# Kernel tuning notes

Hardware: AMD Instinct MI355X
Metric: run time of the kernel (lower is better)

The kernel has to match this reference:

```python
import jax, jax.numpy as jnp
import numpy as np

U, I, NG, D, G, B = 100000, 50000, 20000, 64, 20, 16384
H_GE = (D + 2 * D) // 2  # 96, group_encoder hidden

def setup_inputs() -> dict:
    key = jax.random.key(0)
    ks = jax.random.split(key, 24)
    s = 0.1
    return {
        'group_inputs': jax.random.randint(ks[0], (B,), 0, NG),
        'item_inputs': jax.random.randint(ks[1], (B,), 0, I),
        'group_members': jax.random.randint(ks[2], (NG, G), 0, U),
        'eps': jax.random.normal(ks[3], (B, D), dtype=jnp.float32),
        'user_emb': jax.random.normal(ks[4], (U, D), dtype=jnp.float32) * s,
        'item_emb': jax.random.normal(ks[5], (I, D), dtype=jnp.float32) * s,
        # user_encoder: MLP(D, D, 1) -> Linear(D,D), ReLU, Linear(D,D)
        'ue_w1': jax.random.normal(ks[6], (D, D), dtype=jnp.float32) * s,
        'ue_b1': jnp.zeros((D,), jnp.float32),
        'ue_w2': jax.random.normal(ks[7], (D, D), dtype=jnp.float32) * s,
        'ue_b2': jnp.zeros((D,), jnp.float32),
        # group_encoder: MLP(D, 2D, 1) -> Linear(D,96), ReLU, Linear(96,2D)
        'ge_w1': jax.random.normal(ks[8], (D, H_GE), dtype=jnp.float32) * s,
        'ge_b1': jnp.zeros((H_GE,), jnp.float32),
        'ge_w2': jax.random.normal(ks[9], (H_GE, 2 * D), dtype=jnp.float32) * s,
        'ge_b2': jnp.zeros((2 * D,), jnp.float32),
        # attention: Linear(2D,16), ReLU, Linear(16,1)
        'at_w1': jax.random.normal(ks[10], (2 * D, 16), dtype=jnp.float32) * s,
        'at_b1': jnp.zeros((16,), jnp.float32),
        'at_w2': jax.random.normal(ks[11], (16, 1), dtype=jnp.float32) * s,
        'at_b2': jnp.zeros((1,), jnp.float32),
        # predict: Linear(3D,8), ReLU, Linear(8,1)
        'pr_w1': jax.random.normal(ks[12], (3 * D, 8), dtype=jnp.float32) * s,
        'pr_b1': jnp.zeros((8,), jnp.float32),
        'pr_w2': jax.random.normal(ks[13], (8, 1), dtype=jnp.float32) * s,
        'pr_b2': jnp.zeros((1,), jnp.float32),
    }

def reference(group_inputs, item_inputs, group_members, eps,
              user_emb, item_emb,
              ue_w1, ue_b1, ue_w2, ue_b2,
              ge_w1, ge_b1, ge_w2, ge_b2,
              at_w1, at_b1, at_w2, at_b2,
              pr_w1, pr_b1, pr_w2, pr_b2):
    mem_idx = group_members[group_inputs]              # [B, G]
    me = user_emb[mem_idx]                             # [B, G, D] gather
    # user encoder MLP
    enc = jnp.maximum(me @ ue_w1 + ue_b1, 0) @ ue_w2 + ue_b2
    gz = jnp.maximum(jnp.mean(enc, axis=1), 0)         # [B, D]
    gz = jnp.maximum(gz @ ge_w1 + ge_b1, 0) @ ge_w2 + ge_b2  # [B, 2D]
    z_mu, log_sigma = gz[:, :D], gz[:, D:]
    z_sigma = 0.1 + 0.9 * jax.nn.sigmoid(log_sigma)
    ie = item_emb[item_inputs]                          # [B, D]
    gi = jnp.concatenate([me, jnp.broadcast_to(ie[:, None, :], me.shape)], axis=-1)  # [B, G, 2D]
    score = jnp.maximum(gi @ at_w1 + at_b1, 0) @ at_w2 + at_b2  # [B, G, 1]
    w = jax.nn.softmax(score[..., 0], axis=1)           # [B, G]
    g_att = jnp.einsum('bg,bgd->bd', w, me)             # [B, D]
    ge_full = g_att + z_mu + z_sigma * eps              # sample_z with given eps
    ncf = jnp.concatenate([ge_full * ie, ge_full, ie], axis=-1)  # [B, 3D]
    h = jnp.maximum(ncf @ pr_w1 + pr_b1, 0) @ pr_w2 + pr_b2
    return jax.nn.sigmoid(h)                            # [B, 1]
```

## Files before the change

kernel.cpp:

```cpp
#include <hip/hip_runtime.h>
#include <hip/hip_bf16.h>
#include <math.h>

#define G_   20
#define BT   16

typedef __attribute__((ext_vector_type(8))) short bf8;
typedef __attribute__((ext_vector_type(4))) float f4;

#define FMB  0
#define FAT  10
#define FUE2 12
#define FGE1 20
#define FGE2 32
#define FPR  56
#define FTOT 62

__device__ __forceinline__ unsigned cvt2(float x, float y){
    float2 f; f.x = x; f.y = y;
    __hip_bfloat162 h = __float22bfloat162_rn(f);
    return *reinterpret_cast<unsigned*>(&h);
}
__device__ __forceinline__ unsigned short cvt1(float x){
    __hip_bfloat16 h = __float2bfloat16(x);
    return *reinterpret_cast<unsigned short*>(&h);
}
__device__ __forceinline__ bf8 pack8(float4 a, float4 b){
    union { bf8 v; unsigned u[4]; } t;
    t.u[0] = cvt2(a.x, a.y); t.u[1] = cvt2(a.z, a.w);
    t.u[2] = cvt2(b.x, b.y); t.u[3] = cvt2(b.z, b.w);
    return t.v;
}

__global__ __launch_bounds__(256) void vargr_prep(
    const float* __restrict__ ue_w1, const float* __restrict__ ue_w2,
    const float* __restrict__ ge_w1, const float* __restrict__ ge_w2,
    const float* __restrict__ at_w1, const float* __restrict__ pr_w1,
    unsigned short* __restrict__ ws)
{
    int f = blockIdx.x * 256 + threadIdx.x;
    if (f >= FTOT * 64) return;
    int lane = f & 63, grp = f >> 6;
    int col = lane & 15;
    int q8  = (lane >> 4) * 8;
    float v[8];
    if (grp < FAT){
        int g = grp - FMB; int nt = g >> 1; int k0 = (g & 1)*32 + q8; int c = nt*16 + col;
        #pragma unroll
        for (int q = 0; q < 8; ++q)
            v[q] = (c < 64) ? ue_w1[(k0+q)*64 + c] : at_w1[(k0+q)*16 + (c - 64)];
    } else if (grp < FUE2){
        int g = grp - FAT; int k0 = g*32 + q8;
        #pragma unroll
        for (int q = 0; q < 8; ++q) v[q] = at_w1[(64 + k0 + q)*16 + col];
    } else if (grp < FGE1){
        int g = grp - FUE2; int nt = g >> 1; int k0 = (g & 1)*32 + q8;
        #pragma unroll
        for (int q = 0; q < 8; ++q) v[q] = ue_w2[(k0+q)*64 + nt*16 + col];
    } else if (grp < FGE2){
        int g = grp - FGE1; int nt = g >> 1; int k0 = (g & 1)*32 + q8;
        #pragma unroll
        for (int q = 0; q < 8; ++q) v[q] = ge_w1[(k0+q)*96 + nt*16 + col];
    } else if (grp < FPR){
        int g = grp - FGE2; int nt = g / 3; int k0 = (g % 3)*32 + q8;
        #pragma unroll
        for (int q = 0; q < 8; ++q) v[q] = ge_w2[(k0+q)*128 + nt*16 + col];
    } else {
        int g = grp - FPR; int k0 = g*32 + q8;
        #pragma unroll
        for (int q = 0; q < 8; ++q) v[q] = (col < 8) ? pr_w1[(k0+q)*8 + col] : 0.f;
    }
    union { bf8 b; unsigned u[4]; } t;
    t.u[0] = cvt2(v[0], v[1]); t.u[1] = cvt2(v[2], v[3]);
    t.u[2] = cvt2(v[4], v[5]); t.u[3] = cvt2(v[6], v[7]);
    *reinterpret_cast<bf8*>(ws + (size_t)f * 8) = t.b;
}

__global__ __launch_bounds__(256, 2) void vargr_main(
    const int*   __restrict__ group_inputs,
    const int*   __restrict__ item_inputs,
    const int*   __restrict__ group_members,
    const float* __restrict__ eps,
    const float* __restrict__ user_emb,
    const float* __restrict__ item_emb,
    const float* __restrict__ ue_b1, const float* __restrict__ ue_b2,
    const float* __restrict__ ge_b1, const float* __restrict__ ge_b2,
    const float* __restrict__ at_b1, const float* __restrict__ at_w2,
    const float* __restrict__ at_b2, const float* __restrict__ pr_b1,
    const float* __restrict__ pr_w2, const float* __restrict__ pr_b2,
    const unsigned short* __restrict__ ws,
    float* __restrict__ out)
{
    __shared__ unsigned short xAh[BT*136];
    __shared__ unsigned short xBh[BT*136];
    __shared__ float ieb[BT*68];
    __shared__ float gefb[BT*64];
    __shared__ float wsm[BT*G_];
    __shared__ int   sidx[BT*G_];
    __shared__ float x3u[BT*132];

    const int tid = threadIdx.x;
    const int w = tid >> 6, l = tid & 63;
    const int lq = l >> 4, lr = l & 15;
    const int bbase = blockIdx.x * BT;
    const bf8* wsf = (const bf8*)ws;

    bf8 bfr[5][2];
    #pragma unroll
    for (int nt = 0; nt < 5; ++nt)
        #pragma unroll
        for (int kt = 0; kt < 2; ++kt)
            bfr[nt][kt] = wsf[(FMB + nt*2 + kt)*64 + l];
    bf8 abot0 = wsf[(FAT + 0)*64 + l];
    bf8 abot1 = wsf[(FAT + 1)*64 + l];

    float bias1[4];
    #pragma unroll
    for (int nt = 0; nt < 4; ++nt) bias1[nt] = ue_b1[nt*16 + lr];
    const float aw2  = at_w2[lr];
    const float atb2 = at_b2[0];

    {
        int bb = 4*w + lq;
        int item = item_inputs[bbase + bb];
        ((float4*)(ieb + bb*68))[lr] = ((const float4*)(item_emb + (size_t)item*64))[lr];
    }
    if (l < G_){
        #pragma unroll
        for (int i = 0; i < 4; ++i){
            int bb = 4*w + i;
            int gid = group_inputs[bbase + bb];
            sidx[bb*G_ + l] = group_members[gid*G_ + l];
        }
    }
    __syncthreads();

    float4 r0, r1, r2, r3;
    {
        int sx = sidx[(4*w + (lr >> 2))*G_ + 16 + (lr & 3)];
        const float4* p = (const float4*)(user_emb + (size_t)sx*64) + lq*2;
        r0 = p[0]; r1 = p[1]; r2 = p[8]; r3 = p[9];
    }
    float4 c0, c1, c2, c3;
    {
        int sx = sidx[(4*w + 0)*G_ + lr];
        const float4* p = (const float4*)(user_emb + (size_t)sx*64) + lq*2;
        c0 = p[0]; c1 = p[1]; c2 = p[8]; c3 = p[9];
    }

    f4 tvacc = (f4){0.f, 0.f, 0.f, 0.f};
    #pragma unroll
    for (int kt = 0; kt < 2; ++kt){
        const float* ap = ieb + lr*68 + kt*32 + lq*8;
        bf8 a = pack8(*(const float4*)ap, *(const float4*)(ap + 4));
        tvacc = __builtin_amdgcn_mfma_f32_16x16x32_bf16(a, kt ? abot1 : abot0, tvacc, 0, 0, 0);
    }
    const float atb1 = at_b1[lr];
    float tvi[4];
    #pragma unroll
    for (int i = 0; i < 4; ++i)
        tvi[i] = __shfl(tvacc[i], w*16 + lr) + atb1;

    float rem[4];
    {
        bf8 a0 = pack8(r0, r1);
        bf8 a1 = pack8(r2, r3);
        f4 acc[5];
        #pragma unroll
        for (int nt = 0; nt < 5; ++nt) acc[nt] = (f4){0.f, 0.f, 0.f, 0.f};
        #pragma unroll
        for (int nt = 0; nt < 5; ++nt){
            acc[nt] = __builtin_amdgcn_mfma_f32_16x16x32_bf16(a0, bfr[nt][0], acc[nt], 0, 0, 0);
            acc[nt] = __builtin_amdgcn_mfma_f32_16x16x32_bf16(a1, bfr[nt][1], acc[nt], 0, 0, 0);
        }
        #pragma unroll
        for (int nt = 0; nt < 4; ++nt){
            float rs = 0.f;
            #pragma unroll
            for (int rr = 0; rr < 4; ++rr) rs += fmaxf(acc[nt][rr] + bias1[nt], 0.f);
            rem[nt] = rs;
        }
        float tvq = (lq == 0) ? tvi[0] : (lq == 1) ? tvi[1] : (lq == 2) ? tvi[2] : tvi[3];
        float vv[4];
        #pragma unroll
        for (int rr = 0; rr < 4; ++rr) vv[rr] = fmaxf(acc[4][rr] + tvq, 0.f) * aw2;
        #pragma unroll
        for (int rr = 0; rr < 4; ++rr){
            vv[rr] += __shfl_xor(vv[rr], 1, 16);
            vv[rr] += __shfl_xor(vv[rr], 2, 16);
            vv[rr] += __shfl_xor(vv[rr], 4, 16);
            vv[rr] += __shfl_xor(vv[rr], 8, 16);
        }
        if (lr == 0){
            #pragma unroll
            for (int rr = 0; rr < 4; ++rr)
                wsm[(4*w + lq)*G_ + 16 + rr] = vv[rr] + atb2;
        }
    }

    #pragma unroll
    for (int i = 0; i < 4; ++i){
        float4 n0, n1, n2, n3;
        if (i < 3){
            int sx = sidx[(4*w + i + 1)*G_ + lr];
            const float4* p = (const float4*)(user_emb + (size_t)sx*64) + lq*2;
            n0 = p[0]; n1 = p[1]; n2 = p[8]; n3 = p[9];
        }
        const int bb = 4*w + i;
        bf8 a0 = pack8(c0, c1);
        bf8 a1 = pack8(c2, c3);
        f4 acc[5];
        #pragma unroll
        for (int nt = 0; nt < 5; ++nt) acc[nt] = (f4){0.f, 0.f, 0.f, 0.f};
        #pragma unroll
        for (int nt = 0; nt < 5; ++nt){
            acc[nt] = __builtin_amdgcn_mfma_f32_16x16x32_bf16(a0, bfr[nt][0], acc[nt], 0, 0, 0);
            acc[nt] = __builtin_amdgcn_mfma_f32_16x16x32_bf16(a1, bfr[nt][1], acc[nt], 0, 0, 0);
        }
        #pragma unroll
        for (int nt = 0; nt < 4; ++nt){
            float rs = 0.f;
            #pragma unroll
            for (int rr = 0; rr < 4; ++rr) rs += fmaxf(acc[nt][rr] + bias1[nt], 0.f);
            if (lq == i) rs += rem[nt];
            rs += __shfl_xor(rs, 16);
            rs += __shfl_xor(rs, 32);
            if (lq == nt) xAh[bb*136 + nt*16 + lr] = cvt1(rs * (1.f / G_));
        }
        {
            float vv[4];
            #pragma unroll
            for (int rr = 0; rr < 4; ++rr) vv[rr] = fmaxf(acc[4][rr] + tvi[i], 0.f) * aw2;
            #pragma unroll
            for (int rr = 0; rr < 4; ++rr){
                vv[rr] += __shfl_xor(vv[rr], 1, 16);
                vv[rr] += __shfl_xor(vv[rr], 2, 16);
                vv[rr] += __shfl_xor(vv[rr], 4, 16);
                vv[rr] += __shfl_xor(vv[rr], 8, 16);
            }
            if (lr == 0){
                #pragma unroll
                for (int rr = 0; rr < 4; ++rr)
                    wsm[bb*G_ + 4*lq + rr] = vv[rr] + atb2;
            }
        }
        {
            float sval = (l < G_) ? wsm[bb*G_ + l] : -3.0e38f;
            float mx = sval;
            mx = fmaxf(mx, __shfl_xor(mx, 1, 32));
            mx = fmaxf(mx, __shfl_xor(mx, 2, 32));
            mx = fmaxf(mx, __shfl_xor(mx, 4, 32));
            mx = fmaxf(mx, __shfl_xor(mx, 8, 32));
            mx = fmaxf(mx, __shfl_xor(mx, 16, 32));
            float e = (l < G_) ? expf(sval - mx) : 0.f;
            float sm = e;
            sm += __shfl_xor(sm, 1, 32);
            sm += __shfl_xor(sm, 2, 32);
            sm += __shfl_xor(sm, 4, 32);
            sm += __shfl_xor(sm, 8, 32);
            sm += __shfl_xor(sm, 16, 32);
            if (l < G_) wsm[bb*G_ + l] = e / sm;
        }
        {
            float ga = 0.f;
            #pragma unroll
            for (int g = 0; g < G_; ++g)
                ga += wsm[bb*G_ + g] * user_emb[(size_t)sidx[bb*G_ + g]*64 + l];
            gefb[bb*64 + l] = ga;
        }
        c0 = n0; c1 = n1; c2 = n2; c3 = n3;
    }

    __syncthreads();
    if (w != 0) return;

    float ev[16];
    #pragma unroll
    for (int bb = 0; bb < BT; ++bb)
        ev[bb] = eps[(size_t)(bbase + bb)*64 + l];

    #pragma unroll
    for (int nt = 0; nt < 4; ++nt){
        int col = nt*16 + lr;
        f4 acc = (f4){0.f, 0.f, 0.f, 0.f};
        #pragma unroll
        for (int kt = 0; kt < 2; ++kt){
            bf8 a = *(const bf8*)(xAh + lr*136 + kt*32 + lq*8);
            acc = __builtin_amdgcn_mfma_f32_16x16x32_bf16(a, wsf[(FUE2 + nt*2 + kt)*64 + l], acc, 0, 0, 0);
        }
        float bs = ue_b2[col];
        #pragma unroll
        for (int rr = 0; rr < 4; ++rr)
            xBh[(4*lq + rr)*136 + col] = cvt1(fmaxf(acc[rr] + bs, 0.f));
    }
    #pragma unroll
    for (int t = 0; t < 6; ++t){
        int col = t*16 + lr;
        f4 acc = (f4){0.f, 0.f, 0.f, 0.f};
        #pragma unroll
        for (int kt = 0; kt < 2; ++kt){
            bf8 a = *(const bf8*)(xBh + lr*136 + kt*32 + lq*8);
            acc = __builtin_amdgcn_mfma_f32_16x16x32_bf16(a, wsf[(FGE1 + t*2 + kt)*64 + l], acc, 0, 0, 0);
        }
        float bs = ge_b1[col];
        #pragma unroll
        for (int rr = 0; rr < 4; ++rr)
            xAh[(4*lq + rr)*136 + col] = cvt1(fmaxf(acc[rr] + bs, 0.f));
    }
    #pragma unroll
    for (int t = 0; t < 8; ++t){
        int col = t*16 + lr;
        f4 acc = (f4){0.f, 0.f, 0.f, 0.f};
        #pragma unroll
        for (int kt = 0; kt < 3; ++kt){
            bf8 a = *(const bf8*)(xAh + lr*136 + kt*32 + lq*8);
            acc = __builtin_amdgcn_mfma_f32_16x16x32_bf16(a, wsf[(FGE2 + t*3 + kt)*64 + l], acc, 0, 0, 0);
        }
        float bs = ge_b2[col];
        #pragma unroll
        for (int rr = 0; rr < 4; ++rr)
            x3u[(4*lq + rr)*132 + col] = acc[rr] + bs;
    }

    float gefv[BT];
    #pragma unroll
    for (int bb = 0; bb < BT; ++bb){
        float mu  = x3u[bb*132 + l];
        float sgr = x3u[bb*132 + 64 + l];
        float sg  = 0.1f + 0.9f / (1.f + expf(-sgr));
        gefv[bb] = gefb[bb*64 + l] + mu + sg * ev[bb];
    }
    asm volatile("" ::: "memory");
    unsigned short* ncf = (unsigned short*)x3u;
    #pragma unroll
    for (int bb = 0; bb < BT; ++bb){
        float gef = gefv[bb];
        float iev = ieb[bb*68 + l];
        ncf[bb*200 + l]       = cvt1(gef * iev);
        ncf[bb*200 + 64 + l]  = cvt1(gef);
        ncf[bb*200 + 128 + l] = cvt1(iev);
    }
    {
        f4 acc = (f4){0.f, 0.f, 0.f, 0.f};
        #pragma unroll
        for (int kt = 0; kt < 6; ++kt){
            bf8 a = *(const bf8*)(ncf + lr*200 + kt*32 + lq*8);
            acc = __builtin_amdgcn_mfma_f32_16x16x32_bf16(a, wsf[(FPR + kt)*64 + l], acc, 0, 0, 0);
        }
        float pb1 = (lr < 8) ? pr_b1[lr] : 0.f;
        float pw2 = (lr < 8) ? pr_w2[lr] : 0.f;
        float pb2 = pr_b2[0];
        float vv[4];
        #pragma unroll
        for (int rr = 0; rr < 4; ++rr) vv[rr] = fmaxf(acc[rr] + pb1, 0.f) * pw2;
        #pragma unroll
        for (int rr = 0; rr < 4; ++rr){
            vv[rr] += __shfl_xor(vv[rr], 1, 16);
            vv[rr] += __shfl_xor(vv[rr], 2, 16);
            vv[rr] += __shfl_xor(vv[rr], 4, 16);
            vv[rr] += __shfl_xor(vv[rr], 8, 16);
        }
        if (lr == 0){
            #pragma unroll
            for (int rr = 0; rr < 4; ++rr)
                out[bbase + 4*lq + rr] = 1.f / (1.f + expf(-(vv[rr] + pb2)));
        }
    }
}

extern "C" void kernel_launch(void* const* d_in, const int* in_sizes, int n_in,
                              void* d_out, int out_size, void* d_ws, size_t ws_size,
                              hipStream_t stream) {
    const int*   group_inputs  = (const int*)d_in[0];
    const int*   item_inputs   = (const int*)d_in[1];
    const int*   group_members = (const int*)d_in[2];
    const float* eps           = (const float*)d_in[3];
    const float* user_emb      = (const float*)d_in[4];
    const float* item_emb      = (const float*)d_in[5];
    const float* ue_w1 = (const float*)d_in[6];
    const float* ue_b1 = (const float*)d_in[7];
    const float* ue_w2 = (const float*)d_in[8];
    const float* ue_b2 = (const float*)d_in[9];
    const float* ge_w1 = (const float*)d_in[10];
    const float* ge_b1 = (const float*)d_in[11];
    const float* ge_w2 = (const float*)d_in[12];
    const float* ge_b2 = (const float*)d_in[13];
    const float* at_w1 = (const float*)d_in[14];
    const float* at_b1 = (const float*)d_in[15];
    const float* at_w2 = (const float*)d_in[16];
    const float* at_b2 = (const float*)d_in[17];
    const float* pr_w1 = (const float*)d_in[18];
    const float* pr_b1 = (const float*)d_in[19];
    const float* pr_w2 = (const float*)d_in[20];
    const float* pr_b2 = (const float*)d_in[21];
    float* out = (float*)d_out;
    unsigned short* ws = (unsigned short*)d_ws;

    vargr_prep<<<(FTOT*64 + 255)/256, 256, 0, stream>>>(
        ue_w1, ue_w2, ge_w1, ge_w2, at_w1, pr_w1, ws);

    const int nb = in_sizes[0];
    vargr_main<<<nb / BT, 256, 0, stream>>>(
        group_inputs, item_inputs, group_members, eps, user_emb, item_emb,
        ue_b1, ue_b2, ge_b1, ge_b2, at_b1, at_w2, at_b2, pr_b1, pr_w2, pr_b2,
        ws, out);
}
```

Measured before the change: 40.07 us.

## Split main kernel into gather phase and separate parallel MLP tail kernel

The fused kernel is split in two. The first kernel does the gather, the user-encoder first layer and the attention, and writes the mean hidden, the attended embedding and the item embeddings to workspace. The second kernel runs the group encoder and predict MLPs with every wave active, instead of only wave 0 after a barrier as before. This removes the serial tail where three of four waves sat idle. In exchange it adds an extra launch and round-trips the intermediates through global memory.

Result: slower. 44.72 us (+11.6%).

```diff
diff --git a/kernel.cpp b/kernel.cpp
--- a/kernel.cpp
+++ b/kernel.cpp
@@ -15,6 +15,9 @@
 #define FGE2 32
 #define FPR  56
 #define FTOT 62
+#define HBAR_BOFF  65536u
+#define GEF_BOFF   2162688u
+#define IE_BOFF    6356992u
 
 __device__ __forceinline__ unsigned cvt2(float x, float y){
     float2 f; f.x = x; f.y = y;
@@ -76,28 +79,22 @@
     *reinterpret_cast<bf8*>(ws + (size_t)f * 8) = t.b;
 }
 
-__global__ __launch_bounds__(256, 2) void vargr_main(
+__global__ __launch_bounds__(256, 2) void vargr_phase1(
     const int*   __restrict__ group_inputs,
     const int*   __restrict__ item_inputs,
     const int*   __restrict__ group_members,
-    const float* __restrict__ eps,
     const float* __restrict__ user_emb,
     const float* __restrict__ item_emb,
-    const float* __restrict__ ue_b1, const float* __restrict__ ue_b2,
-    const float* __restrict__ ge_b1, const float* __restrict__ ge_b2,
-    const float* __restrict__ at_b1, const float* __restrict__ at_w2,
-    const float* __restrict__ at_b2, const float* __restrict__ pr_b1,
-    const float* __restrict__ pr_w2, const float* __restrict__ pr_b2,
+    const float* __restrict__ ue_b1, const float* __restrict__ at_b1,
+    const float* __restrict__ at_w2, const float* __restrict__ at_b2,
     const unsigned short* __restrict__ ws,
-    float* __restrict__ out)
+    unsigned short* __restrict__ hbar,
+    float* __restrict__ gef,
+    float* __restrict__ iebuf)
 {
-    __shared__ unsigned short xAh[BT*136];
-    __shared__ unsigned short xBh[BT*136];
     __shared__ float ieb[BT*68];
-    __shared__ float gefb[BT*64];
     __shared__ float wsm[BT*G_];
     __shared__ int   sidx[BT*G_];
-    __shared__ float x3u[BT*132];
 
     const int tid = threadIdx.x;
     const int w = tid >> 6, l = tid & 63;
@@ -123,7 +120,9 @@
     {
         int bb = 4*w + lq;
         int item = item_inputs[bbase + bb];
-        ((float4*)(ieb + bb*68))[lr] = ((const float4*)(item_emb + (size_t)item*64))[lr];
+        float4 v = ((const float4*)(item_emb + (size_t)item*64))[lr];
+        ((float4*)(ieb + bb*68))[lr] = v;
+        ((float4*)(iebuf + (size_t)(bbase + bb)*64))[lr] = v;
     }
     if (l < G_){
         #pragma unroll
@@ -225,7 +224,7 @@
             if (lq == i) rs += rem[nt];
             rs += __shfl_xor(rs, 16);
             rs += __shfl_xor(rs, 32);
-            if (lq == nt) xAh[bb*136 + nt*16 + lr] = cvt1(rs * (1.f / G_));
+            if (lq == nt) hbar[(size_t)(bbase + bb)*64 + nt*16 + lr] = cvt1(rs * (1.f / G_));
         }
         {
             float vv[4];
@@ -266,79 +265,102 @@
             #pragma unroll
             for (int g = 0; g < G_; ++g)
                 ga += wsm[bb*G_ + g] * user_emb[(size_t)sidx[bb*G_ + g]*64 + l];
-            gefb[bb*64 + l] = ga;
+            gef[(size_t)(bbase + bb)*64 + l] = ga;
         }
         c0 = n0; c1 = n1; c2 = n2; c3 = n3;
     }
-
-    __syncthreads();
-    if (w != 0) return;
+}
+
+__global__ __launch_bounds__(128) void vargr_tail(
+    const float* __restrict__ eps,
+    const float* __restrict__ ue_b2, const float* __restrict__ ge_b1,
+    const float* __restrict__ ge_b2, const float* __restrict__ pr_b1,
+    const float* __restrict__ pr_w2, const float* __restrict__ pr_b2,
+    const unsigned short* __restrict__ ws,
+    const unsigned short* __restrict__ hbar,
+    const float* __restrict__ gef,
+    const float* __restrict__ iebuf,
+    float* __restrict__ out)
+{
+    __shared__ unsigned short xA[2][16*136];
+    __shared__ unsigned short xB[2][16*136];
+    __shared__ float x3[2][16*132];
+
+    const int tid = threadIdx.x;
+    const int w = tid >> 6, l = tid & 63;
+    const int lq = l >> 4, lr = l & 15;
+    const int m0 = blockIdx.x * 32 + w * 16;
+    const bf8* wsf = (const bf8*)ws;
 
     float ev[16];
     #pragma unroll
-    for (int bb = 0; bb < BT; ++bb)
-        ev[bb] = eps[(size_t)(bbase + bb)*64 + l];
+    for (int j = 0; j < 16; ++j)
+        ev[j] = eps[(size_t)(m0 + j)*64 + l];
+
+    bf8 ha0 = *(const bf8*)(hbar + (size_t)(m0 + lr)*64 + 0  + lq*8);
+    bf8 ha1 = *(const bf8*)(hbar + (size_t)(m0 + lr)*64 + 32 + lq*8);
 
     #pragma unroll
     for (int nt = 0; nt < 4; ++nt){
         int col = nt*16 + lr;
         f4 acc = (f4){0.f, 0.f, 0.f, 0.f};
-        #pragma unroll
-        for (int kt = 0; kt < 2; ++kt){
-            bf8 a = *(const bf8*)(xAh + lr*136 + kt*32 + lq*8);
-            acc = __builtin_amdgcn_mfma_f32_16x16x32_bf16(a, wsf[(FUE2 + nt*2 + kt)*64 + l], acc, 0, 0, 0);
-        }
+        acc = __builtin_amdgcn_mfma_f32_16x16x32_bf16(ha0, wsf[(FUE2 + nt*2 + 0)*64 + l], acc, 0, 0, 0);
+        acc = __builtin_amdgcn_mfma_f32_16x16x32_bf16(ha1, wsf[(FUE2 + nt*2 + 1)*64 + l], acc, 0, 0, 0);
         float bs = ue_b2[col];
         #pragma unroll
         for (int rr = 0; rr < 4; ++rr)
-            xBh[(4*lq + rr)*136 + col] = cvt1(fmaxf(acc[rr] + bs, 0.f));
-    }
-    #pragma unroll
-    for (int t = 0; t < 6; ++t){
-        int col = t*16 + lr;
-        f4 acc = (f4){0.f, 0.f, 0.f, 0.f};
-        #pragma unroll
-        for (int kt = 0; kt < 2; ++kt){
-            bf8 a = *(const bf8*)(xBh + lr*136 + kt*32 + lq*8);
-            acc = __builtin_amdgcn_mfma_f32_16x16x32_bf16(a, wsf[(FGE1 + t*2 + kt)*64 + l], acc, 0, 0, 0);
-        }
-        float bs = ge_b1[col];
-        #pragma unroll
-        for (int rr = 0; rr < 4; ++rr)
-            xAh[(4*lq + rr)*136 + col] = cvt1(fmaxf(acc[rr] + bs, 0.f));
-    }
-    #pragma unroll
-    for (int t = 0; t < 8; ++t){
-        int col = t*16 + lr;
-        f4 acc = (f4){0.f, 0.f, 0.f, 0.f};
-        #pragma unroll
-        for (int kt = 0; kt < 3; ++kt){
-            bf8 a = *(const bf8*)(xAh + lr*136 + kt*32 + lq*8);
-            acc = __builtin_amdgcn_mfma_f32_16x16x32_bf16(a, wsf[(FGE2 + t*3 + kt)*64 + l], acc, 0, 0, 0);
-        }
-        float bs = ge_b2[col];
-        #pragma unroll
-        for (int rr = 0; rr < 4; ++rr)
-            x3u[(4*lq + rr)*132 + col] = acc[rr] + bs;
-    }
-
-    float gefv[BT];
-    #pragma unroll
-    for (int bb = 0; bb < BT; ++bb){
-        float mu  = x3u[bb*132 + l];
-        float sgr = x3u[bb*132 + 64 + l];
+            xB[w][(4*lq + rr)*136 + col] = cvt1(fmaxf(acc[rr] + bs, 0.f));
+    }
+    {
+        bf8 ga0 = *(const bf8*)(&xB[w][lr*136 + 0  + lq*8]);
+        bf8 ga1 = *(const bf8*)(&xB[w][lr*136 + 32 + lq*8]);
+        #pragma unroll
+        for (int t = 0; t < 6; ++t){
+            int col = t*16 + lr;
+            f4 acc = (f4){0.f, 0.f, 0.f, 0.f};
+            acc = __builtin_amdgcn_mfma_f32_16x16x32_bf16(ga0, wsf[(FGE1 + t*2 + 0)*64 + l], acc, 0, 0, 0);
+            acc = __builtin_amdgcn_mfma_f32_16x16x32_bf16(ga1, wsf[(FGE1 + t*2 + 1)*64 + l], acc, 0, 0, 0);
+            float bs = ge_b1[col];
+            #pragma unroll
+            for (int rr = 0; rr < 4; ++rr)
+                xA[w][(4*lq + rr)*136 + col] = cvt1(fmaxf(acc[rr] + bs, 0.f));
+        }
+    }
+    {
+        bf8 ta0 = *(const bf8*)(&xA[w][lr*136 + 0  + lq*8]);
+        bf8 ta1 = *(const bf8*)(&xA[w][lr*136 + 32 + lq*8]);
+        bf8 ta2 = *(const bf8*)(&xA[w][lr*136 + 64 + lq*8]);
+        #pragma unroll
+        for (int t = 0; t < 8; ++t){
+            int col = t*16 + lr;
+            f4 acc = (f4){0.f, 0.f, 0.f, 0.f};
+            acc = __builtin_amdgcn_mfma_f32_16x16x32_bf16(ta0, wsf[(FGE2 + t*3 + 0)*64 + l], acc, 0, 0, 0);
+            acc = __builtin_amdgcn_mfma_f32_16x16x32_bf16(ta1, wsf[(FGE2 + t*3 + 1)*64 + l], acc, 0, 0, 0);
+            acc = __builtin_amdgcn_mfma_f32_16x16x32_bf16(ta2, wsf[(FGE2 + t*3 + 2)*64 + l], acc, 0, 0, 0);
+            float bs = ge_b2[col];
+            #pragma unroll
+            for (int rr = 0; rr < 4; ++rr)
+                x3[w][(4*lq + rr)*132 + col] = acc[rr] + bs;
+        }
+    }
+
+    float gefv[16];
+    #pragma unroll
+    for (int j = 0; j < 16; ++j){
+        float mu  = x3[w][j*132 + l];
+        float sgr = x3[w][j*132 + 64 + l];
         float sg  = 0.1f + 0.9f / (1.f + expf(-sgr));
-        gefv[bb] = gefb[bb*64 + l] + mu + sg * ev[bb];
+        gefv[j] = gef[(size_t)(m0 + j)*64 + l] + mu + sg * ev[j];
     }
     asm volatile("" ::: "memory");
-    unsigned short* ncf = (unsigned short*)x3u;
-    #pragma unroll
-    for (int bb = 0; bb < BT; ++bb){
-        float gef = gefv[bb];
-        float iev = ieb[bb*68 + l];
-        ncf[bb*200 + l]       = cvt1(gef * iev);
-        ncf[bb*200 + 64 + l]  = cvt1(gef);
-        ncf[bb*200 + 128 + l] = cvt1(iev);
+    unsigned short* ncf = (unsigned short*)&x3[w][0];
+    #pragma unroll
+    for (int j = 0; j < 16; ++j){
+        float g  = gefv[j];
+        float ie = iebuf[(size_t)(m0 + j)*64 + l];
+        ncf[j*200 + l]       = cvt1(g * ie);
+        ncf[j*200 + 64 + l]  = cvt1(g);
+        ncf[j*200 + 128 + l] = cvt1(ie);
     }
     {
         f4 acc = (f4){0.f, 0.f, 0.f, 0.f};
@@ -363,7 +385,7 @@
         if (lr == 0){
             #pragma unroll
             for (int rr = 0; rr < 4; ++rr)
-                out[bbase + 4*lq + rr] = 1.f / (1.f + expf(-(vv[rr] + pb2)));
+                out[m0 + 4*lq + rr] = 1.f / (1.f + expf(-(vv[rr] + pb2)));
         }
     }
 }
@@ -396,12 +418,19 @@
     float* out = (float*)d_out;
     unsigned short* ws = (unsigned short*)d_ws;
 
+    unsigned short* hbar  = (unsigned short*)((char*)d_ws + HBAR_BOFF);
+    float*          gef   = (float*)((char*)d_ws + GEF_BOFF);
+    float*          iebuf = (float*)((char*)d_ws + IE_BOFF);
+
     vargr_prep<<<(FTOT*64 + 255)/256, 256, 0, stream>>>(
         ue_w1, ue_w2, ge_w1, ge_w2, at_w1, pr_w1, ws);
 
     const int nb = in_sizes[0];
-    vargr_main<<<nb / BT, 256, 0, stream>>>(
-        group_inputs, item_inputs, group_members, eps, user_emb, item_emb,
-        ue_b1, ue_b2, ge_b1, ge_b2, at_b1, at_w2, at_b2, pr_b1, pr_w2, pr_b2,
-        ws, out);
-}
+    vargr_phase1<<<nb / BT, 256, 0, stream>>>(
+        group_inputs, item_inputs, group_members, user_emb, item_emb,
+        ue_b1, at_b1, at_w2, at_b2, ws, hbar, gef, iebuf);
+
+    vargr_tail<<<nb / 32, 128, 0, stream>>>(
+        eps, ue_b2, ge_b1, ge_b2, pr_b1, pr_w2, pr_b2,
+        ws, hbar, gef, iebuf, out);
+}
```
